# Optimization experiments

Hardware: AMD Instinct MI355X
Metric: run time of the kernel (lower is better)

## Reference

```python
import jax, jax.numpy as jnp
import numpy as np

V = 10000   # vocab size
H = 768     # HIDDEN_SIZE
B = 8       # batch
S = 512     # padded seq len
L = 8       # TRANSFORMER_LAYERS
EPS = 1e-5  # torch LayerNorm default eps


def setup_inputs() -> dict:
    key = jax.random.key(0)
    ks = jax.random.split(key, 16)
    init = lambda k, shape: jax.random.normal(k, shape, jnp.float32) * 0.02
    x = jax.random.randint(ks[0], (B, S), 0, V)
    # full-length sequences: avoids NaN from the original's softmax(dim=1) over
    # fully -inf padded columns (same behavior as torch for this input)
    lengths = jnp.full((B,), S, dtype=jnp.int32)
    return {
        'x': x,
        'lengths': lengths,
        'emb_w': init(ks[1], (V, H)),
        'Wq': init(ks[2], (L, H, H)), 'bq': jnp.zeros((L, H), jnp.float32),
        'Wk': init(ks[3], (L, H, H)), 'bk': jnp.zeros((L, H), jnp.float32),
        'Wv': init(ks[4], (L, H, H)), 'bv': jnp.zeros((L, H), jnp.float32),
        'W1': init(ks[5], (L, H, H)), 'b1': jnp.zeros((L, H), jnp.float32),
        'W2': init(ks[6], (L, H, H)), 'b2': jnp.zeros((L, H), jnp.float32),
        'g1': jnp.ones((L, H), jnp.float32), 'be1': jnp.zeros((L, H), jnp.float32),
        'g2': jnp.ones((L, H), jnp.float32), 'be2': jnp.zeros((L, H), jnp.float32),
        'fc_w': init(ks[7], (H, H)), 'fc_b': jnp.zeros((H,), jnp.float32),
    }


def _layernorm(x, g, b):
    m = jnp.mean(x, axis=-1, keepdims=True)
    v = jnp.mean(jnp.square(x - m), axis=-1, keepdims=True)
    return (x - m) * jax.lax.rsqrt(v + EPS) * g + b


def _pos_encoding(seq, dim):
    pos = jnp.arange(seq, dtype=jnp.float32)[:, None]
    div = jnp.exp(jnp.arange(0, dim, 2, dtype=jnp.float32) * (-np.log(10000.0) / dim))
    ang = pos * div[None, :]                                  # [S, H/2]
    return jnp.stack([jnp.sin(ang), jnp.cos(ang)], axis=-1).reshape(seq, dim)


def reference(x, lengths, emb_w, Wq, bq, Wk, bk, Wv, bv, W1, b1, W2, b2,
              g1, be1, g2, be2, fc_w, fc_b):
    z = emb_w[x] + _pos_encoding(S, H)[None]                  # [B,S,H]
    causal = jnp.tril(jnp.ones((S, S), bool))                 # [S,S]
    valid = jnp.arange(S)[None, :] < lengths[:, None]         # [B,S]
    mask = causal[None] & valid[:, None, :] & valid[:, :, None]  # [B,S,S]
    scale = 1.0 / jnp.sqrt(jnp.float32(H))
    for i in range(L):
        q = z @ Wq[i] + bq[i]
        k = z @ Wk[i] + bk[i]
        v = z @ Wv[i] + bv[i]
        scores = jnp.einsum('bqh,bkh->bqk', q, k) * scale
        scores = jnp.where(mask, scores, -jnp.inf)
        # NOTE: original code applies softmax over dim=1 (query axis) — faithful
        atten = jax.nn.softmax(scores, axis=1)
        out = jnp.einsum('bqk,bkh->bqh', atten, v)
        o1 = _layernorm(z + out, g1[i], be1[i])               # eval: dropout=identity
        mid = jax.nn.relu(o1 @ W1[i] + b1[i]) @ W2[i] + b2[i]
        z = _layernorm(mid + o1, g2[i], be2[i])
    zf = z @ fc_w + fc_b                                      # [B,S,H]
    logits = jnp.einsum('bsh,vh->bsv', zf, emb_w)             # [B,S,V]
    return jax.nn.softmax(logits, axis=-1)
```

## Files before the change

kernel.cpp:

```cpp
#include <hip/hip_runtime.h>
#include <math.h>

typedef unsigned int   u32;
typedef unsigned short u16;
typedef __attribute__((ext_vector_type(8))) short bf16x8;
typedef __attribute__((ext_vector_type(4))) float f32x4;
typedef __attribute__((ext_vector_type(4))) unsigned short u16x4;
typedef __attribute__((ext_vector_type(8))) unsigned short u16x8;

#define HID   768
#define SEQ   512
#define BATCH 8
#define LAYERS 8
#define VOC   10000
#define NROWS (BATCH*SEQ)
#define NH    ((long long)NROWS*HID)
#define SS8   ((long long)BATCH*SEQ*SEQ)
#define EPSLN 1e-5f
#define WSZ   ((long long)HID*HID)

__device__ __forceinline__ u16 f2bf(float f) {
    u32 u = __builtin_bit_cast(u32, f);
    return (u16)((u + 0x7fffu + ((u >> 16) & 1u)) >> 16);
}
__device__ __forceinline__ float bf2f(u16 h) {
    return __builtin_bit_cast(float, (u32)h << 16);
}

__device__ __forceinline__ void async16(u16* lds, const u16* g) {
    __builtin_amdgcn_global_load_lds(
        (const __attribute__((address_space(1))) u32*)g,
        (__attribute__((address_space(3))) u32*)lds, 16, 0, 0);
}

__global__ __launch_bounds__(256) void embed_kernel(
    const int* __restrict__ x, const float* __restrict__ emb,
    float* __restrict__ Z, u16* __restrict__ Zh)
{
    const int row = blockIdx.x;
    const int s   = row & (SEQ - 1);
    const int tok = x[row];
    const long long base  = (long long)row * HID;
    const long long ebase = (long long)tok * HID;
    const float coef = -0.0239852613853544f;
    #pragma unroll
    for (int j = 0; j < 3; ++j) {
        const int h = threadIdx.x + 256 * j;
        const int i = h >> 1;
        const float ang = (float)s * expf((float)i * coef);
        const float pe  = (h & 1) ? cosf(ang) : sinf(ang);
        const float v = emb[ebase + h] + pe;
        Z[base + h]  = v;
        Zh[base + h] = f2bf(v);
    }
}

__global__ __launch_bounds__(256) void convert_emb(
    const float* __restrict__ e, u16* __restrict__ eh)
{
    const long long i = ((long long)blockIdx.x * 256 + threadIdx.x) * 4;
    const float4 v = *(const float4*)&e[i];
    u16x4 p;
    p[0] = f2bf(v.x); p[1] = f2bf(v.y); p[2] = f2bf(v.z); p[3] = f2bf(v.w);
    *(u16x4*)&eh[i] = p;
}

__global__ __launch_bounds__(256) void transp_all(
    const float* __restrict__ Wq, const float* __restrict__ Wk,
    const float* __restrict__ Wv, const float* __restrict__ W1,
    const float* __restrict__ W2, const float* __restrict__ fcw,
    u16* __restrict__ WT)
{
    __shared__ u16 tile[32][34];
    const int z = blockIdx.z;
    const float* src;
    long long doff;
    if (z < 40) {
        const int lyr = z / 5, idx = z % 5;
        const float* bases[5] = {Wq, Wk, Wv, W1, W2};
        src  = bases[idx] + (long long)lyr * WSZ;
        doff = ((long long)lyr * 5 + idx) * WSZ;
    } else {
        src = fcw; doff = 40LL * WSZ;
    }
    u16* D = WT + doff;
    const int n0 = blockIdx.x * 32, k0 = blockIdx.y * 32;
    const int c = threadIdx.x & 31, r0 = threadIdx.x >> 5;
    #pragma unroll
    for (int p = 0; p < 4; ++p)
        tile[r0 + 8*p][c] = f2bf(src[(long long)(k0 + r0 + 8*p) * HID + n0 + c]);
    __syncthreads();
    #pragma unroll
    for (int p = 0; p < 4; ++p)
        D[(long long)(n0 + r0 + 8*p) * HID + k0 + c] = tile[c][r0 + 8*p];
}

__global__ void pack_bias_all(const float* __restrict__ bq,
                              const float* __restrict__ bk,
                              const float* __restrict__ bv,
                              float* __restrict__ dst)
{
    const int part = blockIdx.x, l = blockIdx.y, h = threadIdx.x;
    const float* src = part == 0 ? bq : (part == 1 ? bk : bv);
    dst[((long long)l*3 + part) * HID + h] = src[(long long)l*HID + h];
}

template<bool XISM, bool VSPLIT>
__global__ __launch_bounds__(256) void gemm_big(
    const u16* __restrict__ A, const u16* __restrict__ B,
    u16* __restrict__ Cp, int ldc, int N, int K,
    const float* __restrict__ bias, u16* __restrict__ vt)
{
    __shared__ u16 As[2][128 * 64];
    __shared__ u16 Bs[2][128 * 64];
    const int m0 = (XISM ? blockIdx.x : blockIdx.y) * 128;
    const int n0 = (XISM ? blockIdx.y : blockIdx.x) * 128;
    const int t = threadIdx.x, w = t >> 6, l = t & 63;
    const int wm = (w >> 1) * 64, wn = (w & 1) * 64;

    f32x4 acc[4][4];
    #pragma unroll
    for (int mi = 0; mi < 4; ++mi)
        #pragma unroll
        for (int ni = 0; ni < 4; ++ni) acc[mi][ni] = (f32x4){0.f,0.f,0.f,0.f};

    auto stage = [&](int buf, int kt) {
        #pragma unroll
        for (int r = 0; r < 4; ++r) {
            const int f = r * 256 + t;
            const int row = f >> 3, j = f & 7;
            async16(&As[buf][f * 8],
                    A + (long long)(m0 + row) * K + kt + ((j ^ (row & 7)) << 3));
        }
        #pragma unroll
        for (int r = 0; r < 4; ++r) {
            const int f = r * 256 + t;
            const int row = f >> 3, j = f & 7;
            int gr = n0 + row; gr = gr < N ? gr : N - 1;
            async16(&Bs[buf][f * 8],
                    B + (long long)gr * K + kt + ((j ^ (row & 7)) << 3));
        }
    };
    const int fr = l & 15, fk = l >> 4;
    auto compute = [&](int cur) {
        #pragma unroll
        for (int ks = 0; ks < 2; ++ks) {
            bf16x8 af[4], bfr[4];
            #pragma unroll
            for (int mi = 0; mi < 4; ++mi) {
                const int row = wm + mi*16 + fr;
                af[mi] = *(const bf16x8*)
                    &As[cur][row * 64 + (((ks*4 + fk) ^ (row & 7)) << 3)];
            }
            #pragma unroll
            for (int ni = 0; ni < 4; ++ni) {
                const int row = wn + ni*16 + fr;
                bfr[ni] = *(const bf16x8*)
                    &Bs[cur][row * 64 + (((ks*4 + fk) ^ (row & 7)) << 3)];
            }
            __builtin_amdgcn_s_setprio(1);
            #pragma unroll
            for (int mi = 0; mi < 4; ++mi)
                #pragma unroll
                for (int ni = 0; ni < 4; ++ni)
                    acc[mi][ni] = __builtin_amdgcn_mfma_f32_16x16x32_bf16(
                        af[mi], bfr[ni], acc[mi][ni], 0, 0, 0);
            __builtin_amdgcn_s_setprio(0);
        }
    };

    const int NS = K >> 6;
    stage(0, 0);
    for (int tt = 0; tt < NS; ++tt) {
        if (tt + 1 < NS) {
            stage((tt + 1) & 1, (tt + 1) << 6);
            asm volatile("s_waitcnt vmcnt(8)\n\ts_barrier" ::: "memory");
        } else {
            asm volatile("s_waitcnt vmcnt(0)\n\ts_barrier" ::: "memory");
        }
        compute(tt & 1);
        asm volatile("s_barrier" ::: "memory");
    }

    const int fq = l >> 4;
    #pragma unroll
    for (int ni = 0; ni < 4; ++ni) {
        const int col = n0 + wn + ni*16 + fr;
        if (col >= N) continue;
        const float bv = bias ? bias[col] : 0.f;
        #pragma unroll
        for (int mi = 0; mi < 4; ++mi) {
            const int row0 = m0 + wm + mi*16 + fq*4;
            if constexpr (VSPLIT) {
                if (col < 1536) {
                    #pragma unroll
                    for (int v = 0; v < 4; ++v)
                        Cp[(long long)(row0 + v) * ldc + col] =
                            f2bf(acc[mi][ni][v] + bv);
                } else {
                    const int b9 = row0 >> 9, s9 = row0 & 511;
                    u16x4 pk;
                    #pragma unroll
                    for (int v = 0; v < 4; ++v)
                        pk[v] = f2bf(acc[mi][ni][v] + bv);
                    *(u16x4*)&vt[((long long)b9 * HID + (col - 1536)) * SEQ + s9] = pk;
                }
            } else {
                #pragma unroll
                for (int v = 0; v < 4; ++v)
                    Cp[(long long)(row0 + v) * ldc + col] =
                        f2bf(acc[mi][ni][v] + bv);
            }
        }
    }
}

template<bool RELU, bool OUT_BF16>
__global__ __launch_bounds__(128) void gemm_small(
    const u16* __restrict__ A, int lda, long long sA,
    const u16* __restrict__ B, int ldb, long long sB,
    void* __restrict__ Cp, int ldc, long long sC,
    int N, int K, const float* __restrict__ bias, float alpha)
{
    __shared__ u16 As[2][64 * 64];
    __shared__ u16 Bs[2][64 * 64];
    const int bz = blockIdx.z;
    const int n0 = blockIdx.x * 64;
    const int m0 = blockIdx.y * 64;
    const int t = threadIdx.x, w = t >> 6, l = t & 63;
    const int srow = l >> 3;
    const int skof = ((l & 7) ^ srow) * 8;
    const int wm = w * 32;
    A += sA * bz; B += sB * bz;

    f32x4 acc[2][4];
    #pragma unroll
    for (int mi = 0; mi < 2; ++mi)
        #pragma unroll
        for (int ni = 0; ni < 4; ++ni) acc[mi][ni] = (f32x4){0.f,0.f,0.f,0.f};

    auto stage = [&](int buf, int k0) {
        #pragma unroll
        for (int r = 0; r < 4; ++r) {
            const int seg = w * 4 + r;
            const int row = seg * 8 + srow;
            async16(&As[buf][seg * 512],
                    A + (long long)(m0 + row) * lda + (k0 + skof));
        }
        #pragma unroll
        for (int r = 0; r < 4; ++r) {
            const int seg = w * 4 + r;
            const int row = seg * 8 + srow;
            async16(&Bs[buf][seg * 512],
                    B + (long long)(n0 + row) * ldb + (k0 + skof));
        }
    };
    const int fr = l & 15, fkb = l >> 4;
    auto compute = [&](int cur) {
        #pragma unroll
        for (int ks = 0; ks < 2; ++ks) {
            const int ps = ((ks * 4 + fkb) ^ (fr & 7)) * 8;
            bf16x8 af[2], bfv[4];
            #pragma unroll
            for (int mi = 0; mi < 2; ++mi)
                af[mi] = *(const bf16x8*)&As[cur][(wm + mi*16 + fr) * 64 + ps];
            #pragma unroll
            for (int ni = 0; ni < 4; ++ni)
                bfv[ni] = *(const bf16x8*)&Bs[cur][(ni*16 + fr) * 64 + ps];
            #pragma unroll
            for (int mi = 0; mi < 2; ++mi)
                #pragma unroll
                for (int ni = 0; ni < 4; ++ni)
                    acc[mi][ni] = __builtin_amdgcn_mfma_f32_16x16x32_bf16(
                        af[mi], bfv[ni], acc[mi][ni], 0, 0, 0);
        }
    };

    const int NS = K >> 6;
    stage(0, 0);
    for (int tt = 0; tt < NS; ++tt) {
        if (tt + 1 < NS) {
            stage((tt + 1) & 1, (tt + 1) << 6);
            asm volatile("s_waitcnt vmcnt(8)\n\ts_barrier" ::: "memory");
        } else {
            asm volatile("s_waitcnt vmcnt(0)\n\ts_barrier" ::: "memory");
        }
        compute(tt & 1);
        asm volatile("s_barrier" ::: "memory");
    }

    float* Cf = (float*)Cp + sC * bz;
    u16*   Ch = (u16*)Cp + sC * bz;
    const int fq = l >> 4;
    #pragma unroll
    for (int ni = 0; ni < 4; ++ni) {
        const int col = n0 + ni*16 + fr;
        const float bv = bias ? bias[col] : 0.f;
        #pragma unroll
        for (int mi = 0; mi < 2; ++mi) {
            const int row0 = m0 + wm + mi*16 + fq*4;
            #pragma unroll
            for (int v = 0; v < 4; ++v) {
                float val = alpha * acc[mi][ni][v] + bv;
                if (RELU) val = fmaxf(val, 0.f);
                if (OUT_BF16) Ch[(long long)(row0 + v) * ldc + col] = f2bf(val);
                else          Cf[(long long)(row0 + v) * ldc + col] = val;
            }
        }
    }
}

__global__ __launch_bounds__(256) void gemm_conv(
    const u16* __restrict__ A, const float* __restrict__ Bf,
    u16* __restrict__ C)
{
    __shared__ u16 As[128 * 32];
    __shared__ u16 Bs[128 * 32];
    const int m0 = blockIdx.x * 128;
    const int n0 = blockIdx.y * 128;
    const int t = threadIdx.x, w = t >> 6, l = t & 63;
    const int lrow = l >> 2, lk8 = (l & 3) * 8;
    const int wm = (w >> 1) * 64, wn = (w & 1) * 64;
    f32x4 acc[4][4];
    #pragma unroll
    for (int mi = 0; mi < 4; ++mi)
        #pragma unroll
        for (int ni = 0; ni < 4; ++ni) acc[mi][ni] = (f32x4){0.f,0.f,0.f,0.f};

    for (int k0 = 0; k0 < HID; k0 += 32) {
        #pragma unroll
        for (int r = 0; r < 2; ++r) {
            const int seg = w * 2 + r;
            async16(&As[seg * 512],
                    A + (long long)(m0 + seg*16 + lrow) * HID + (k0 + lk8));
        }
        #pragma unroll
        for (int r = 0; r < 2; ++r) {
            const int flat = r * 2048 + t * 8;
            int row = n0 + (flat >> 5);
            row = row < VOC ? row : VOC - 1;
            const float* g = Bf + (long long)row * HID + (k0 + (flat & 31));
            const float4 v0 = *(const float4*)g;
            const float4 v1 = *(const float4*)(g + 4);
            bf16x8 hv;
            hv[0]=(short)f2bf(v0.x); hv[1]=(short)f2bf(v0.y);
            hv[2]=(short)f2bf(v0.z); hv[3]=(short)f2bf(v0.w);
            hv[4]=(short)f2bf(v1.x); hv[5]=(short)f2bf(v1.y);
            hv[6]=(short)f2bf(v1.z); hv[7]=(short)f2bf(v1.w);
            *(bf16x8*)&Bs[flat] = hv;
        }
        __syncthreads();
        const int fr = l & 15, fk = (l >> 4) * 8;
        bf16x8 af[4], bfr[4];
        #pragma unroll
        for (int mi = 0; mi < 4; ++mi)
            af[mi] = *(const bf16x8*)&As[(wm + mi*16 + fr) * 32 + fk];
        #pragma unroll
        for (int ni = 0; ni < 4; ++ni)
            bfr[ni] = *(const bf16x8*)&Bs[(wn + ni*16 + fr) * 32 + fk];
        #pragma unroll
        for (int mi = 0; mi < 4; ++mi)
            #pragma unroll
            for (int ni = 0; ni < 4; ++ni)
                acc[mi][ni] = __builtin_amdgcn_mfma_f32_16x16x32_bf16(
                    af[mi], bfr[ni], acc[mi][ni], 0, 0, 0);
        __syncthreads();
    }
    const int fr = l & 15, fq = l >> 4;
    #pragma unroll
    for (int ni = 0; ni < 4; ++ni) {
        const int col = n0 + wn + ni*16 + fr;
        if (col >= VOC) continue;
        #pragma unroll
        for (int mi = 0; mi < 4; ++mi) {
            const int row0 = m0 + wm + mi*16 + fq*4;
            #pragma unroll
            for (int v = 0; v < 4; ++v)
                C[(long long)(row0 + v) * (2*VOC) + col] = f2bf(acc[mi][ni][v]);
        }
    }
}

__global__ __launch_bounds__(256) void softmax_q_kernel(
    const float* __restrict__ sc, u16* __restrict__ att,
    const int* __restrict__ lengths)
{
    const int b  = blockIdx.x;
    const int k0 = blockIdx.y * 16;
    const int tx = threadIdx.x & 15;
    const int ty = threadIdx.x >> 4;
    const int c  = k0 + tx;
    const int len = lengths[b];
    const float* base  = sc  + (long long)b * SEQ * SEQ;
    u16*         obase = att + (long long)b * SEQ * SEQ;
    const bool cvalid = (c < len);

    float vals[32];
    float m = -3.0e38f, ssum = 0.f;
    #pragma unroll
    for (int i = 0; i < 32; ++i) {
        const int q = ty + 16 * i;
        float xv = -3.0e38f;
        if (cvalid && c <= q && q < len)
            xv = base[(long long)q * SEQ + c];
        vals[i] = xv;
        if (xv > m) { ssum = ssum * __expf(m - xv) + 1.f; m = xv; }
        else if (xv > -3.0e38f) { ssum += __expf(xv - m); }
    }
    __shared__ float ms[16][17], ss[16][17];
    ms[ty][tx] = m; ss[ty][tx] = ssum;
    __syncthreads();
    if (ty == 0) {
        float M = ms[0][tx];
        #pragma unroll
        for (int r = 1; r < 16; ++r) M = fmaxf(M, ms[r][tx]);
        float Sx = 0.f;
        #pragma unroll
        for (int r = 0; r < 16; ++r) Sx += ss[r][tx] * __expf(ms[r][tx] - M);
        ms[0][tx] = M; ss[0][tx] = Sx;
    }
    __syncthreads();
    const float M   = ms[0][tx];
    const float den = ss[0][tx];
    const float inv = (den > 0.f) ? 1.f / den : 0.f;
    #pragma unroll
    for (int i = 0; i < 32; ++i) {
        const int q = ty + 16 * i;
        obase[(long long)q * SEQ + c] = f2bf(__expf(vals[i] - M) * inv);
    }
}

__global__ __launch_bounds__(256) void ln_add_kernel(
    const float* __restrict__ Xa, const float* __restrict__ Xb,
    float* __restrict__ O, u16* __restrict__ Oh,
    const float* __restrict__ g, const float* __restrict__ be)
{
    const int row = blockIdx.x * 4 + (threadIdx.x >> 6);
    const int l = threadIdx.x & 63;
    const long long base = (long long)row * HID;
    float x[12];
    #pragma unroll
    for (int c = 0; c < 3; ++c) {
        const int off = c * 256 + l * 4;
        const float4 a = *(const float4*)&Xa[base + off];
        const float4 b = *(const float4*)&Xb[base + off];
        x[c*4+0] = a.x + b.x; x[c*4+1] = a.y + b.y;
        x[c*4+2] = a.z + b.z; x[c*4+3] = a.w + b.w;
    }
    float s = 0.f;
    #pragma unroll
    for (int i = 0; i < 12; ++i) s += x[i];
    #pragma unroll
    for (int o = 32; o; o >>= 1) s += __shfl_xor(s, o, 64);
    const float mean = s * (1.f / HID);
    float v = 0.f;
    #pragma unroll
    for (int i = 0; i < 12; ++i) { const float d = x[i] - mean; v += d * d; }
    #pragma unroll
    for (int o = 32; o; o >>= 1) v += __shfl_xor(v, o, 64);
    const float rs = rsqrtf(v * (1.f / HID) + EPSLN);
    #pragma unroll
    for (int c = 0; c < 3; ++c) {
        const int off = c * 256 + l * 4;
        const float4 gg = *(const float4*)&g[off];
        const float4 bb = *(const float4*)&be[off];
        float4 y;
        y.x = (x[c*4+0] - mean) * rs * gg.x + bb.x;
        y.y = (x[c*4+1] - mean) * rs * gg.y + bb.y;
        y.z = (x[c*4+2] - mean) * rs * gg.z + bb.z;
        y.w = (x[c*4+3] - mean) * rs * gg.w + bb.w;
        *(float4*)&O[base + off] = y;
        u16x4 p;
        p[0] = f2bf(y.x); p[1] = f2bf(y.y); p[2] = f2bf(y.z); p[3] = f2bf(y.w);
        *(u16x4*)&Oh[base + off] = p;
    }
}

__global__ __launch_bounds__(256) void softmax_v_kernel(float* __restrict__ out)
{
    __shared__ float row[VOC];
    __shared__ float rm[4], rs_[4];
    const long long obase = (long long)blockIdx.x * VOC;
    const u16* lg = (const u16*)out + 2 * obase + VOC;
    const int t = threadIdx.x;
    float m = -3.0e38f, s = 0.f;
    for (int i = t * 8; i < VOC; i += 2048) {
        const u16x8 h8 = *(const u16x8*)&lg[i];
        #pragma unroll
        for (int j = 0; j < 8; ++j) {
            const float xv = bf2f(h8[j]);
            row[i + j] = xv;
            const float d = xv - m;
            if (d > 0.f) { s = s * __expf(-d) + 1.f; m = xv; }
            else         { s += __expf(d); }
        }
    }
    #pragma unroll
    for (int o = 32; o; o >>= 1) {
        const float om = __shfl_down(m, o, 64), os = __shfl_down(s, o, 64);
        const float M = fmaxf(m, om);
        s = s * __expf(m - M) + os * __expf(om - M);
        m = M;
    }
    if ((t & 63) == 0) { rm[t >> 6] = m; rs_[t >> 6] = s; }
    __syncthreads();
    const float M = fmaxf(fmaxf(rm[0], rm[1]), fmaxf(rm[2], rm[3]));
    const float S = rs_[0]*__expf(rm[0]-M) + rs_[1]*__expf(rm[1]-M)
                  + rs_[2]*__expf(rm[2]-M) + rs_[3]*__expf(rm[3]-M);
    const float inv = 1.f / S;
    for (int i = t * 4; i < VOC; i += 1024) {
        float4 v = *(const float4*)&row[i];
        v.x = __expf(v.x - M) * inv;
        v.y = __expf(v.y - M) * inv;
        v.z = __expf(v.z - M) * inv;
        v.w = __expf(v.w - M) * inv;
        *(float4*)&out[obase + i] = v;
    }
}

extern "C" void kernel_launch(void* const* d_in, const int* in_sizes, int n_in,
                              void* d_out, int out_size, void* d_ws, size_t ws_size,
                              hipStream_t stream)
{
    const int*   x    = (const int*)  d_in[0];
    const int*   lens = (const int*)  d_in[1];
    const float* emb  = (const float*)d_in[2];
    const float* Wq   = (const float*)d_in[3];
    const float* bq   = (const float*)d_in[4];
    const float* Wk   = (const float*)d_in[5];
    const float* bk   = (const float*)d_in[6];
    const float* Wv   = (const float*)d_in[7];
    const float* bv   = (const float*)d_in[8];
    const float* W1   = (const float*)d_in[9];
    const float* b1   = (const float*)d_in[10];
    const float* W2   = (const float*)d_in[11];
    const float* b2   = (const float*)d_in[12];
    const float* g1   = (const float*)d_in[13];
    const float* be1  = (const float*)d_in[14];
    const float* g2   = (const float*)d_in[15];
    const float* be2  = (const float*)d_in[16];
    const float* fcw  = (const float*)d_in[17];
    const float* fcb  = (const float*)d_in[18];

    float* out = (float*)d_out;
    float* Zb     = out;
    float* O1f    = Zb + NH;
    float* M2f    = O1f + NH;
    float* SCORES = M2f + NH;
    float* BQKV   = SCORES + SS8;
    u16* ub   = (u16*)(BQKV + (long long)LAYERS * 2304);
    u16* Zbh  = ub;  ub += NH;
    u16* QKVh = ub;  ub += (long long)NROWS * 1536;
    u16* ATTB = ub;  ub += SS8;
    u16* Vt   = ub;  ub += NH;
    u16* O1h  = ub;  ub += NH;
    u16* M1h  = ub;  ub += NH;
    u16* WT   = ub;  ub += 41LL * WSZ;

    u16* ZFh = (u16*)d_ws;
    u16* EH  = ZFh + NH;
    const bool ehpath = ws_size >= (size_t)((NH + (long long)VOC * HID) * 2);
    u16* LOGH = (u16*)out + VOC;

    const float scale = 1.0f / sqrtf((float)HID);
    const dim3 blk(256), blk128(128);

    embed_kernel<<<NROWS, blk, 0, stream>>>(x, emb, Zb, Zbh);
    transp_all<<<dim3(24, 24, 41), blk, 0, stream>>>(Wq, Wk, Wv, W1, W2, fcw, WT);
    pack_bias_all<<<dim3(3, LAYERS), dim3(768), 0, stream>>>(bq, bk, bv, BQKV);
    if (ehpath) convert_emb<<<7500, blk, 0, stream>>>(emb, EH);

    for (int l = 0; l < LAYERS; ++l) {
        const u16* wl = WT + (long long)l * 5 * WSZ;

        gemm_big<false, true><<<dim3(18, 32), blk, 0, stream>>>(
            Zbh, wl, QKVh, 1536, 2304, HID,
            BQKV + (long long)l * 2304, Vt);

        gemm_small<false, false><<<dim3(8, 8, BATCH), blk128, 0, stream>>>(
            QKVh, 1536, (long long)SEQ * 1536,
            QKVh + 768, 1536, (long long)SEQ * 1536,
            SCORES, SEQ, (long long)SEQ * SEQ,
            512, HID, nullptr, scale);

        softmax_q_kernel<<<dim3(BATCH, SEQ/16), blk, 0, stream>>>(SCORES, ATTB, lens);

        gemm_small<false, false><<<dim3(12, 8, BATCH), blk128, 0, stream>>>(
            ATTB, SEQ, (long long)SEQ * SEQ,
            Vt, SEQ, (long long)HID * SEQ,
            O1f, HID, (long long)SEQ * HID,
            768, SEQ, nullptr, 1.0f);

        ln_add_kernel<<<NROWS/4, blk, 0, stream>>>(Zb, O1f, O1f, O1h,
                                                   g1 + l*HID, be1 + l*HID);
        gemm_small<true, true><<<dim3(12, 64), blk128, 0, stream>>>(
            O1h, HID, 0, wl + 3*WSZ, HID, 0, M1h, HID, 0,
            768, HID, b1 + l*HID, 1.0f);
        gemm_small<false, false><<<dim3(12, 64), blk128, 0, stream>>>(
            M1h, HID, 0, wl + 4*WSZ, HID, 0, M2f, HID, 0,
            768, HID, b2 + l*HID, 1.0f);
        ln_add_kernel<<<NROWS/4, blk, 0, stream>>>(M2f, O1f, Zb, Zbh,
                                                   g2 + l*HID, be2 + l*HID);
    }

    gemm_small<false, true><<<dim3(12, 64), blk128, 0, stream>>>(
        Zbh, HID, 0, WT + 40LL*WSZ, HID, 0, ZFh, HID, 0,
        768, HID, fcb, 1.0f);

    if (ehpath) {
        gemm_big<true, false><<<dim3(32, 79), blk, 0, stream>>>(
            ZFh, EH, LOGH, 2*VOC, VOC, HID, nullptr, nullptr);
    } else {
        gemm_conv<<<dim3(32, 79), blk, 0, stream>>>(ZFh, emb, LOGH);
    }

    softmax_v_kernel<<<NROWS, blk, 0, stream>>>(out);
}
```

Measured before the change: 1.126 ms.

## Switch GEMM shared-memory tiles to k-slot-major layout and halve big-GEMM K tile

The shared-memory layout in both GEMM kernels changes from row-major with an XOR swizzle to a k-slot-major layout, where each 16-byte k chunk of every row is stored contiguously by row. This removes the swizzle arithmetic and is meant to give conflict-free fragment reads. The big GEMM also drops its K tile from 64 to 32, which halves LDS use to allow more occupancy and removes the setprio hints. In exchange it runs twice as many barrier-synchronised iterations, and the global loads become less contiguous per row, with each thread fetching 16 bytes from a different row.

Result: slower. 1.475 ms (+31.0%).

```diff
diff --git a/kernel.cpp b/kernel.cpp
--- a/kernel.cpp
+++ b/kernel.cpp
@@ -111,8 +111,8 @@
     u16* __restrict__ Cp, int ldc, int N, int K,
     const float* __restrict__ bias, u16* __restrict__ vt)
 {
-    __shared__ u16 As[2][128 * 64];
-    __shared__ u16 Bs[2][128 * 64];
+    __shared__ u16 As[2][128 * 32];
+    __shared__ u16 Bs[2][128 * 32];
     const int m0 = (XISM ? blockIdx.x : blockIdx.y) * 128;
     const int n0 = (XISM ? blockIdx.y : blockIdx.x) * 128;
     const int t = threadIdx.x, w = t >> 6, l = t & 63;
@@ -126,55 +126,44 @@
 
     auto stage = [&](int buf, int kt) {
         #pragma unroll
-        for (int r = 0; r < 4; ++r) {
-            const int f = r * 256 + t;
-            const int row = f >> 3, j = f & 7;
-            async16(&As[buf][f * 8],
-                    A + (long long)(m0 + row) * K + kt + ((j ^ (row & 7)) << 3));
-        }
-        #pragma unroll
-        for (int r = 0; r < 4; ++r) {
-            const int f = r * 256 + t;
-            const int row = f >> 3, j = f & 7;
+        for (int r = 0; r < 2; ++r) {
+            const int c = r * 256 + t;
+            const int row = c & 127, slot = c >> 7;
+            async16(&As[buf][c * 8],
+                    A + (long long)(m0 + row) * K + kt + slot * 8);
+        }
+        #pragma unroll
+        for (int r = 0; r < 2; ++r) {
+            const int c = r * 256 + t;
+            const int row = c & 127, slot = c >> 7;
             int gr = n0 + row; gr = gr < N ? gr : N - 1;
-            async16(&Bs[buf][f * 8],
-                    B + (long long)gr * K + kt + ((j ^ (row & 7)) << 3));
+            async16(&Bs[buf][c * 8],
+                    B + (long long)gr * K + kt + slot * 8);
         }
     };
     const int fr = l & 15, fk = l >> 4;
     auto compute = [&](int cur) {
-        #pragma unroll
-        for (int ks = 0; ks < 2; ++ks) {
-            bf16x8 af[4], bfr[4];
+        bf16x8 af[4], bfr[4];
+        #pragma unroll
+        for (int mi = 0; mi < 4; ++mi)
+            af[mi] = *(const bf16x8*)&As[cur][(fk * 128 + wm + mi*16 + fr) * 8];
+        #pragma unroll
+        for (int ni = 0; ni < 4; ++ni)
+            bfr[ni] = *(const bf16x8*)&Bs[cur][(fk * 128 + wn + ni*16 + fr) * 8];
+        #pragma unroll
+        for (int mi = 0; mi < 4; ++mi)
             #pragma unroll
-            for (int mi = 0; mi < 4; ++mi) {
-                const int row = wm + mi*16 + fr;
-                af[mi] = *(const bf16x8*)
-                    &As[cur][row * 64 + (((ks*4 + fk) ^ (row & 7)) << 3)];
-            }
-            #pragma unroll
-            for (int ni = 0; ni < 4; ++ni) {
-                const int row = wn + ni*16 + fr;
-                bfr[ni] = *(const bf16x8*)
-                    &Bs[cur][row * 64 + (((ks*4 + fk) ^ (row & 7)) << 3)];
-            }
-            __builtin_amdgcn_s_setprio(1);
-            #pragma unroll
-            for (int mi = 0; mi < 4; ++mi)
-                #pragma unroll
-                for (int ni = 0; ni < 4; ++ni)
-                    acc[mi][ni] = __builtin_amdgcn_mfma_f32_16x16x32_bf16(
-                        af[mi], bfr[ni], acc[mi][ni], 0, 0, 0);
-            __builtin_amdgcn_s_setprio(0);
-        }
+            for (int ni = 0; ni < 4; ++ni)
+                acc[mi][ni] = __builtin_amdgcn_mfma_f32_16x16x32_bf16(
+                    af[mi], bfr[ni], acc[mi][ni], 0, 0, 0);
     };
 
-    const int NS = K >> 6;
+    const int NS = K >> 5;
     stage(0, 0);
     for (int tt = 0; tt < NS; ++tt) {
         if (tt + 1 < NS) {
-            stage((tt + 1) & 1, (tt + 1) << 6);
-            asm volatile("s_waitcnt vmcnt(8)\n\ts_barrier" ::: "memory");
+            stage((tt + 1) & 1, (tt + 1) << 5);
+            asm volatile("s_waitcnt vmcnt(4)\n\ts_barrier" ::: "memory");
         } else {
             asm volatile("s_waitcnt vmcnt(0)\n\ts_barrier" ::: "memory");
         }
@@ -228,8 +217,6 @@
     const int n0 = blockIdx.x * 64;
     const int m0 = blockIdx.y * 64;
     const int t = threadIdx.x, w = t >> 6, l = t & 63;
-    const int srow = l >> 3;
-    const int skof = ((l & 7) ^ srow) * 8;
     const int wm = w * 32;
     A += sA * bz; B += sB * bz;
 
@@ -242,31 +229,31 @@
     auto stage = [&](int buf, int k0) {
         #pragma unroll
         for (int r = 0; r < 4; ++r) {
-            const int seg = w * 4 + r;
-            const int row = seg * 8 + srow;
-            async16(&As[buf][seg * 512],
-                    A + (long long)(m0 + row) * lda + (k0 + skof));
+            const int c = r * 128 + t;
+            const int row = c & 63, slot = c >> 6;
+            async16(&As[buf][c * 8],
+                    A + (long long)(m0 + row) * lda + k0 + slot * 8);
         }
         #pragma unroll
         for (int r = 0; r < 4; ++r) {
-            const int seg = w * 4 + r;
-            const int row = seg * 8 + srow;
-            async16(&Bs[buf][seg * 512],
-                    B + (long long)(n0 + row) * ldb + (k0 + skof));
+            const int c = r * 128 + t;
+            const int row = c & 63, slot = c >> 6;
+            async16(&Bs[buf][c * 8],
+                    B + (long long)(n0 + row) * ldb + k0 + slot * 8);
         }
     };
     const int fr = l & 15, fkb = l >> 4;
     auto compute = [&](int cur) {
         #pragma unroll
         for (int ks = 0; ks < 2; ++ks) {
-            const int ps = ((ks * 4 + fkb) ^ (fr & 7)) * 8;
+            const int slot = ks * 4 + fkb;
             bf16x8 af[2], bfv[4];
             #pragma unroll
             for (int mi = 0; mi < 2; ++mi)
-                af[mi] = *(const bf16x8*)&As[cur][(wm + mi*16 + fr) * 64 + ps];
+                af[mi] = *(const bf16x8*)&As[cur][(slot * 64 + wm + mi*16 + fr) * 8];
             #pragma unroll
             for (int ni = 0; ni < 4; ++ni)
-                bfv[ni] = *(const bf16x8*)&Bs[cur][(ni*16 + fr) * 64 + ps];
+                bfv[ni] = *(const bf16x8*)&Bs[cur][(slot * 64 + ni*16 + fr) * 8];
             #pragma unroll
             for (int mi = 0; mi < 2; ++mi)
                 #pragma unroll
```
